# Kernel optimization log

Measured on AMD Instinct MI355X. Metric: run time of the kernel, lower is better.

The kernel has to match this reference:

```python
import jax, jax.numpy as jnp
import numpy as np

B, S, D, H, DFF = 4, 2048, 768, 12, 3072
DH = D // H  # 64
EPS = 1e-5
SQRT_DK = float(np.sqrt(DH))


def layer_norm(x, gamma, beta):
    mu = jnp.mean(x, axis=-1, keepdims=True)
    var = jnp.mean((x - mu) ** 2, axis=-1, keepdims=True)
    return (x - mu) / jnp.sqrt(var + EPS) * gamma + beta


def attention_block(x, Wq, Wv, gamma, beta, mask):
    # NOTE: faithful to source quirks: k and v BOTH come from the V projection
    # (self.K is unused), and softmax is over dim=2 (the QUERY axis) as in
    # nn.Softmax(dim=2) applied to a (B, H, Sq, Sk) tensor.
    b, s, d = x.shape
    q = (x @ Wq).reshape(b, s, H, DH).transpose(0, 2, 1, 3)   # (B,H,S,DH)
    kv = (x @ Wv).reshape(b, s, H, DH).transpose(0, 2, 1, 3)  # (B,H,S,DH)
    w = jnp.einsum('bhqd,bhkd->bhqk', q, kv) / SQRT_DK        # (B,H,S,S)
    w = jnp.where(mask, -1e9, w)
    score = jax.nn.softmax(w, axis=2)  # dim=2 quirk (query axis)
    o = jnp.einsum('bhqk,bhkd->bhqd', score, kv)
    o = o.transpose(0, 2, 1, 3).reshape(b, s, d)
    return layer_norm(o + x, gamma, beta)


def feed_forward(x, W1, b1, W2, b2, gamma, beta):
    h = jax.nn.relu(x @ W1 + b1)
    return layer_norm(h @ W2 + b2 + x, gamma, beta)


def setup_inputs() -> dict:
    key = jax.random.key(0)
    ks = jax.random.split(key, 12)
    std = 1.0 / np.sqrt(D)
    x = jax.random.normal(ks[0], (B, S, D), dtype=jnp.float32)
    # causal mask: True = masked
    mask = jnp.triu(jnp.ones((S, S), dtype=bool), k=1)[None, None]
    return {
        'x': x,
        'mask': mask,
        'Wq1': jax.random.normal(ks[1], (D, D), jnp.float32) * std,
        'Wv1': jax.random.normal(ks[2], (D, D), jnp.float32) * std,
        'g1': jnp.ones((D,), jnp.float32),
        'be1': jnp.zeros((D,), jnp.float32),
        'Wq2': jax.random.normal(ks[3], (D, D), jnp.float32) * std,
        'Wv2': jax.random.normal(ks[4], (D, D), jnp.float32) * std,
        'g2': jnp.ones((D,), jnp.float32),
        'be2': jnp.zeros((D,), jnp.float32),
        'Wf1': jax.random.normal(ks[5], (D, DFF), jnp.float32) * std,
        'bf1': jnp.zeros((DFF,), jnp.float32),
        'Wf2': jax.random.normal(ks[6], (DFF, D), jnp.float32) * (1.0 / np.sqrt(DFF)),
        'bf2': jnp.zeros((D,), jnp.float32),
        'gf': jnp.ones((D,), jnp.float32),
        'bef': jnp.zeros((D,), jnp.float32),
    }


def reference(x, mask, Wq1, Wv1, g1, be1, Wq2, Wv2, g2, be2,
              Wf1, bf1, Wf2, bf2, gf, bef):
    x = attention_block(x, Wq1, Wv1, g1, be1, mask)
    # second block: mask is zeroed in the source (no masking)
    x = attention_block(x, Wq2, Wv2, g2, be2, jnp.zeros_like(mask))
    x = feed_forward(x, Wf1, bf1, Wf2, bf2, gf, bef)
    return x
```

## Files before the change

kernel.cpp:

```cpp
#include <hip/hip_runtime.h>

typedef __attribute__((ext_vector_type(8))) short short8;
typedef __attribute__((ext_vector_type(4))) float floatx4;
typedef __attribute__((ext_vector_type(4))) unsigned short ushort4v;

#define H_ 12
#define S_ 2048
#define D_ 768
#define DFF_ 3072
#define DH_ 64
#define BH_ 48
#define M_ 8192
#define QSCALE 0.180336880f

#if defined(__has_builtin)
#if __has_builtin(__builtin_amdgcn_exp2f)
#define EXP2V(x) __builtin_amdgcn_exp2f(x)
#endif
#if __has_builtin(__builtin_amdgcn_logf)
#define LOG2V(x) __builtin_amdgcn_logf(x)
#endif
#endif
#ifndef EXP2V
#define EXP2V(x) exp2f(x)
#endif
#ifndef LOG2V
#define LOG2V(x) log2f(x)
#endif

__device__ __forceinline__ unsigned short f2bf(float f) {
  union { float f; unsigned int u; } a; a.f = f;
  return (unsigned short)((a.u + 0x7FFFu + ((a.u >> 16) & 1u)) >> 16);
}
__device__ __forceinline__ unsigned int cvtpk_bf16(float lo, float hi) {
  unsigned int u;
  asm("v_cvt_pk_bf16_f32 %0, %1, %2" : "=v"(u) : "v"(lo), "v"(hi));
  return u;
}

__device__ __forceinline__ void glds16(const void* g, void* l) {
  __builtin_amdgcn_global_load_lds(
      (const __attribute__((address_space(1))) void*)(unsigned long long)(size_t)g,
      (__attribute__((address_space(3))) void*)(unsigned int)(size_t)l, 16, 0, 0);
}
__device__ __forceinline__ void glds4(const void* g, void* l) {
  __builtin_amdgcn_global_load_lds(
      (const __attribute__((address_space(1))) void*)(unsigned long long)(size_t)g,
      (__attribute__((address_space(3))) void*)(unsigned int)(size_t)l, 4, 0, 0);
}

__device__ __forceinline__ int swz8(int lin, int nwg) {
  return (lin & 7) * (nwg >> 3) + (lin >> 3);
}

__global__ __launch_bounds__(256) void cvt_bf16(const float* __restrict__ in,
                                                unsigned short* __restrict__ out) {
  size_t i = ((size_t)blockIdx.x * 256 + threadIdx.x) * 4;
  floatx4 v = *reinterpret_cast<const floatx4*>(in + i);
  ushort4v o;
  o[0] = f2bf(v[0]); o[1] = f2bf(v[1]); o[2] = f2bf(v[2]); o[3] = f2bf(v[3]);
  *reinterpret_cast<ushort4v*>(out + i) = o;
}

__global__ __launch_bounds__(256) void wtrans(const float* __restrict__ W,
                                              unsigned short* __restrict__ Wt,
                                              int K, int N) {
  __shared__ float t[64][65];
  const int n0 = blockIdx.x * 64, k0 = blockIdx.y * 64;
  const int tid = threadIdx.x;
#pragma unroll
  for (int i = 0; i < 16; ++i) {
    int idx = tid + 256 * i;
    int kl = idx >> 6, nl = idx & 63;
    t[kl][nl] = W[(size_t)(k0 + kl) * N + n0 + nl];
  }
  __syncthreads();
#pragma unroll
  for (int i = 0; i < 16; ++i) {
    int idx = tid + 256 * i;
    int nl = idx >> 6, kl = idx & 63;
    Wt[(size_t)(n0 + nl) * K + k0 + kl] = f2bf(t[kl][nl]);
  }
}

__global__ __launch_bounds__(256) void kvtrans(const unsigned short* __restrict__ KVb,
                                               unsigned short* __restrict__ KVTb,
                                               unsigned short* __restrict__ kfb) {
  __shared__ unsigned short t[64][72];
  const int kt = blockIdx.x;
  const int kk0 = kt * 64;
  const int bh = blockIdx.y, b = bh / H_, h = bh % H_;
  const size_t xbase = ((size_t)b * S_) * D_ + h * DH_;
  const int tid = threadIdx.x;
#pragma unroll
  for (int i = 0; i < 16; ++i) {
    int idx = tid + 256 * i;
    int kl = idx >> 6, d = idx & 63;
    t[kl][d] = KVb[xbase + (size_t)(kk0 + kl) * D_ + d];
  }
  __syncthreads();
  const size_t tb = (size_t)bh * DH_ * S_;
#pragma unroll
  for (int i = 0; i < 16; ++i) {
    int idx = tid + 256 * i;
    int d = idx >> 6, kl = idx & 63;
    KVTb[tb + (size_t)d * S_ + kk0 + kl] = t[kl][d];
  }
  const size_t obase = ((size_t)bh * 32 + kt) * 4096;
#pragma unroll
  for (int i = 0; i < 2; ++i) {
    int idx = tid + 256 * i;
    int fi = idx >> 6, ll = idx & 63;
    int kkf = fi >> 1, s = fi & 1;
    short8 v =
        *reinterpret_cast<const short8*>(&t[kkf * 16 + (ll & 15)][s * 32 + (ll >> 4) * 8]);
    *reinterpret_cast<short8*>(&kfb[obase + (size_t)fi * 512 + ll * 8]) = v;
  }
}

template <int EPI, int OUTBF>
__global__ __launch_bounds__(256, 2) void gemm128(const unsigned short* __restrict__ A,
                                                  const unsigned short* __restrict__ Bt,
                                                  const float* __restrict__ bias,
                                                  float scale, void* __restrict__ C0,
                                                  void* __restrict__ C1,
                                                  int M, int N, int K, int lda) {
  __shared__ unsigned short As[128 * 64];
  __shared__ unsigned short Bs[128 * 64];
  const int tid = threadIdx.x;
  const int l = tid & 63, w = tid >> 6;
  const int wm = w >> 1, wn = w & 1;
  const int lrow = l & 15, lk = l >> 4;
  int lin = (blockIdx.z * gridDim.y + blockIdx.y) * gridDim.x + blockIdx.x;
  int nwg = gridDim.x * gridDim.y * gridDim.z;
  int s = swz8(lin, nwg);
  int xt = s % gridDim.x;
  int rest = s / gridDim.x;
  int yt = rest % gridDim.y;
  int zt = rest / gridDim.y;
  const unsigned short* Ao = A + (size_t)zt * K;
  const unsigned short* Bo = Bt + (size_t)zt * K;
  const int m0 = yt * 128, n0 = xt * 128;
  floatx4 acc[4][4] = {};
  for (int k0 = 0; k0 < K; k0 += 64) {
    __syncthreads();
#pragma unroll
    for (int i = 0; i < 4; ++i) {
      int idx = w * 64 + i * 256 + l;
      int row = idx >> 3, c8 = idx & 7;
      int sc = (c8 ^ (row & 7)) << 3;
      glds16(Ao + (size_t)(m0 + row) * lda + k0 + sc, As + (size_t)(w * 64 + i * 256) * 8);
      glds16(Bo + (size_t)(n0 + row) * lda + k0 + sc, Bs + (size_t)(w * 64 + i * 256) * 8);
    }
    __syncthreads();
#pragma unroll
    for (int ks = 0; ks < 2; ++ks) {
      short8 af[4], bfr[4];
#pragma unroll
      for (int f = 0; f < 4; ++f) {
        int ar = wm * 64 + f * 16 + lrow;
        af[f] = *reinterpret_cast<const short8*>(
            &As[ar * 64 + (((ks * 4 + lk) ^ (ar & 7)) << 3)]);
        int br = wn * 64 + f * 16 + lrow;
        bfr[f] = *reinterpret_cast<const short8*>(
            &Bs[br * 64 + (((ks * 4 + lk) ^ (br & 7)) << 3)]);
      }
#pragma unroll
      for (int fm = 0; fm < 4; ++fm)
#pragma unroll
        for (int fn = 0; fn < 4; ++fn)
          acc[fm][fn] =
              __builtin_amdgcn_mfma_f32_16x16x32_bf16(af[fm], bfr[fn], acc[fm][fn], 0, 0, 0);
    }
  }
#pragma unroll
  for (int fm = 0; fm < 4; ++fm) {
#pragma unroll
    for (int fn = 0; fn < 4; ++fn) {
      int col = n0 + wn * 64 + fn * 16 + lrow;
#pragma unroll
      for (int r = 0; r < 4; ++r) {
        int row = m0 + wm * 64 + fm * 16 + lk * 4 + r;
        float v = acc[fm][fn][r];
        if (EPI == 3) {
          if (col < 768)
            ((unsigned short*)C0)[(size_t)row * 768 + col] = f2bf(v * scale);
          else
            ((unsigned short*)C1)[(size_t)row * 768 + col - 768] = f2bf(v);
        } else {
          v = v * scale + ((EPI > 0) ? bias[col] : 0.0f);
          if (EPI == 1) v = fmaxf(v, 0.0f);
          void* Cz = zt ? C1 : C0;
          if (OUTBF) ((unsigned short*)Cz)[(size_t)row * N + col] = f2bf(v);
          else ((float*)Cz)[(size_t)row * N + col] = v;
        }
      }
    }
  }
}

template <bool CAUSAL>
__global__ __launch_bounds__(256, 4) void colsum(const unsigned short* __restrict__ Qb,
                                                 const unsigned short* __restrict__ kfb,
                                                 float* __restrict__ lnl) {
  __shared__ float lred[4][64];
  const int tid = threadIdx.x;
  const int l = tid & 63, w = tid >> 6;
  const int lrow = l & 15, lk = l >> 4;
  const int sw = swz8(blockIdx.x, 32 * BH_);
  const int bh = sw >> 5, kt = sw & 31;
  const int kk0 = kt * 64;
  const int b = bh / H_, h = bh % H_;
  const size_t xbase = ((size_t)b * S_) * D_ + h * DH_;
  const unsigned short* kfT = kfb + ((size_t)bh * 32 + kt) * 4096;
  short8 bkv[4][2];
#pragma unroll
  for (int kkf = 0; kkf < 4; ++kkf)
#pragma unroll
    for (int s = 0; s < 2; ++s)
      bkv[kkf][s] =
          *reinterpret_cast<const short8*>(&kfT[(size_t)(kkf * 2 + s) * 512 + l * 8]);
  float lrun[4] = {0.0f, 0.0f, 0.0f, 0.0f};
  const int qbase = CAUSAL ? kk0 : 0;
  const int ntiles = (S_ - qbase) >> 4;
  short8 aqn[2];
  if (w < ntiles) {
    const int q0 = qbase + w * 16;
#pragma unroll
    for (int s = 0; s < 2; ++s)
      aqn[s] = *reinterpret_cast<const short8*>(
          &Qb[xbase + (size_t)(q0 + lrow) * D_ + s * 32 + lk * 8]);
  }
  for (int t = w; t < ntiles; t += 4) {
    const int q0 = qbase + t * 16;
    const bool maskt = CAUSAL && (q0 < kk0 + 64);
    short8 aq0 = aqn[0], aq1 = aqn[1];
    if (t + 4 < ntiles) {
      const int qn = qbase + (t + 4) * 16;
#pragma unroll
      for (int s = 0; s < 2; ++s)
        aqn[s] = *reinterpret_cast<const short8*>(
            &Qb[xbase + (size_t)(qn + lrow) * D_ + s * 32 + lk * 8]);
    }
#pragma unroll
    for (int kkf = 0; kkf < 4; ++kkf) {
      floatx4 sf = {};
      sf = __builtin_amdgcn_mfma_f32_16x16x32_bf16(aq0, bkv[kkf][0], sf, 0, 0, 0);
      sf = __builtin_amdgcn_mfma_f32_16x16x32_bf16(aq1, bkv[kkf][1], sf, 0, 0, 0);
      const int kkg = kk0 + kkf * 16 + lrow;
      float lacc = 0.0f;
      if (maskt) {
#pragma unroll
        for (int r = 0; r < 4; ++r) {
          int qg = q0 + lk * 4 + r;
          lacc += (kkg <= qg) ? EXP2V(sf[r]) : 0.0f;
        }
      } else {
#pragma unroll
        for (int r = 0; r < 4; ++r) lacc += EXP2V(sf[r]);
      }
      lrun[kkf] += lacc;
    }
  }
#pragma unroll
  for (int kkf = 0; kkf < 4; ++kkf) {
    float lv = lrun[kkf];
    lv += __shfl_xor(lv, 16, 64);
    lv += __shfl_xor(lv, 32, 64);
    if (l < 16) lred[w][kkf * 16 + l] = lv;
  }
  __syncthreads();
  if (tid < 64) {
    float lv = lred[0][tid] + lred[1][tid] + lred[2][tid] + lred[3][tid];
    lnl[(size_t)bh * S_ + kk0 + tid] = -LOG2V(lv);
  }
}

template <bool CAUSAL>
__global__ __launch_bounds__(256, 3) void attnpv(const unsigned short* __restrict__ Qb,
                                                 const unsigned short* __restrict__ kfb,
                                                 const unsigned short* __restrict__ KVTb,
                                                 const float* __restrict__ lnl,
                                                 float* __restrict__ Opre) {
  __shared__ unsigned short kvts[2][64 * 64];
  __shared__ float slnl[2][4][64];
  __shared__ unsigned short ps[4][32 * 64];
  const int tid = threadIdx.x;
  const int l = tid & 63, w = tid >> 6;
  const int lrow = l & 15, lk = l >> 4;
  const int sw = swz8(blockIdx.x, 16 * BH_);
  const int bh = sw >> 4, qtr = sw & 15;
  const int qt = CAUSAL ? (15 - qtr) : qtr;
  const int q0 = qt * 128;
  const int wr = w * 32;
  const int b = bh / H_, h = bh % H_;
  const size_t xbase = ((size_t)b * S_) * D_ + h * DH_;
  const size_t tbase = (size_t)bh * DH_ * S_;
  const float* lnlb = lnl + (size_t)bh * S_;
  const unsigned short* kfB = kfb + (size_t)bh * 32 * 4096;

  auto STAGE = [&](int buf, int t) {
    const int kk0 = t * 64;
#pragma unroll
    for (int i = 0; i < 2; ++i) {
      int idx = w * 64 + i * 256 + l;
      int row = idx >> 3, c8 = idx & 7;
      int sc = (c8 ^ (row & 7)) << 3;
      glds16(KVTb + tbase + (size_t)row * S_ + kk0 + sc,
             &kvts[buf][(size_t)(w * 64 + i * 256) * 8]);
    }
    glds4(lnlb + kk0 + l, &slnl[buf][w][0]);
  };

  short8 aq[2][2];
#pragma unroll
  for (int fm = 0; fm < 2; ++fm)
#pragma unroll
    for (int s = 0; s < 2; ++s)
      aq[fm][s] = *reinterpret_cast<const short8*>(
          &Qb[xbase + (size_t)(q0 + wr + fm * 16 + lrow) * D_ + s * 32 + lk * 8]);
  floatx4 ao[2][4] = {};
  const int nkk = CAUSAL ? 2 * (qt + 1) : (S_ / 64);

  STAGE(0, 0);
  int cur = 0;
  for (int t = 0; t < nkk; ++t) {
    const int kk0 = t * 64;
    const bool maskt = CAUSAL && (kk0 + 64 > q0);
    short8 kc[8];
#pragma unroll
    for (int fi = 0; fi < 8; ++fi)
      kc[fi] =
          *reinterpret_cast<const short8*>(&kfB[((size_t)t * 8 + fi) * 512 + l * 8]);
    if (t + 1 < nkk) {
      STAGE(cur ^ 1, t + 1);
      __builtin_amdgcn_sched_barrier(0);
      asm volatile("s_waitcnt vmcnt(11)" ::: "memory");
    } else {
      __builtin_amdgcn_sched_barrier(0);
      asm volatile("s_waitcnt vmcnt(8)" ::: "memory");
    }
    __builtin_amdgcn_s_barrier();
    __builtin_amdgcn_sched_barrier(0);
#pragma unroll
    for (int kkf = 0; kkf < 4; ++kkf) {
      const floatx4 nl4 =
          *reinterpret_cast<const floatx4*>(&slnl[cur][w][kkf * 16 + lk * 4]);
      const int kkbase = kk0 + kkf * 16 + lk * 4;
#pragma unroll
      for (int fm = 0; fm < 2; ++fm) {
        floatx4 sf = nl4;
        sf = __builtin_amdgcn_mfma_f32_16x16x32_bf16(kc[kkf * 2 + 0], aq[fm][0], sf, 0, 0, 0);
        sf = __builtin_amdgcn_mfma_f32_16x16x32_bf16(kc[kkf * 2 + 1], aq[fm][1], sf, 0, 0, 0);
        float p0 = EXP2V(sf[0]);
        float p1 = EXP2V(sf[1]);
        float p2 = EXP2V(sf[2]);
        float p3 = EXP2V(sf[3]);
        if (maskt) {
          const int qg = q0 + wr + fm * 16 + lrow;
          p0 = (kkbase + 0 <= qg) ? p0 : 0.0f;
          p1 = (kkbase + 1 <= qg) ? p1 : 0.0f;
          p2 = (kkbase + 2 <= qg) ? p2 : 0.0f;
          p3 = (kkbase + 3 <= qg) ? p3 : 0.0f;
        }
        unsigned int u0 = cvtpk_bf16(p0, p1);
        unsigned int u1 = cvtpk_bf16(p2, p3);
        const int rowq = fm * 16 + lrow;
        unsigned short* pb =
            &ps[w][rowq * 64 + ((((kkf << 1) + (lk >> 1)) ^ (lrow & 7)) << 3) +
                   ((lk & 1) << 2)];
        *reinterpret_cast<unsigned int*>(pb) = u0;
        *reinterpret_cast<unsigned int*>(pb + 2) = u1;
      }
    }
    short8 pa[2][2];
#pragma unroll
    for (int fm = 0; fm < 2; ++fm)
#pragma unroll
      for (int s2 = 0; s2 < 2; ++s2)
        pa[fm][s2] = *reinterpret_cast<const short8*>(
            &ps[w][(fm * 16 + lrow) * 64 + (((s2 * 4 + lk) ^ (lrow & 7)) << 3)]);
    __builtin_amdgcn_s_setprio(1);
#pragma unroll
    for (int dn = 0; dn < 4; ++dn) {
#pragma unroll
      for (int s2 = 0; s2 < 2; ++s2) {
        const int br2 = dn * 16 + lrow;
        short8 bv = *reinterpret_cast<const short8*>(
            &kvts[cur][br2 * 64 + (((s2 * 4 + lk) ^ (br2 & 7)) << 3)]);
#pragma unroll
        for (int fm = 0; fm < 2; ++fm)
          ao[fm][dn] =
              __builtin_amdgcn_mfma_f32_16x16x32_bf16(pa[fm][s2], bv, ao[fm][dn], 0, 0, 0);
      }
    }
    __builtin_amdgcn_s_setprio(0);
    __builtin_amdgcn_sched_barrier(0);
    __builtin_amdgcn_s_barrier();
    __builtin_amdgcn_sched_barrier(0);
    cur ^= 1;
  }
#pragma unroll
  for (int fm = 0; fm < 2; ++fm)
#pragma unroll
    for (int dn = 0; dn < 4; ++dn)
#pragma unroll
      for (int r = 0; r < 4; ++r)
        Opre[xbase + (size_t)(q0 + wr + fm * 16 + lk * 4 + r) * D_ + dn * 16 + lrow] =
            ao[fm][dn][r];
}

template <bool WRITEBF, bool TWO, bool BIAS>
__global__ __launch_bounds__(256) void ln_kernel(const float* __restrict__ pre,
                                                 const float* __restrict__ pre2,
                                                 const float* __restrict__ bias,
                                                 const float* __restrict__ res,
                                                 const float* __restrict__ gam,
                                                 const float* __restrict__ bet,
                                                 float* __restrict__ outf,
                                                 unsigned short* __restrict__ outb) {
  const int w = threadIdx.x >> 6, l = threadIdx.x & 63;
  const int row = blockIdx.x * 4 + w;
  const size_t base = (size_t)row * D_;
  floatx4 v[3];
  float s = 0.0f;
#pragma unroll
  for (int j = 0; j < 3; ++j) {
    int i = j * 256 + l * 4;
    floatx4 t = *reinterpret_cast<const floatx4*>(&pre[base + i]);
    floatx4 rv = *reinterpret_cast<const floatx4*>(&res[base + i]);
#pragma unroll
    for (int e = 0; e < 4; ++e) t[e] += rv[e];
    if (TWO) {
      floatx4 t2 = *reinterpret_cast<const floatx4*>(&pre2[base + i]);
#pragma unroll
      for (int e = 0; e < 4; ++e) t[e] += t2[e];
    }
    if (BIAS) {
      floatx4 bv = *reinterpret_cast<const floatx4*>(&bias[i]);
#pragma unroll
      for (int e = 0; e < 4; ++e) t[e] += bv[e];
    }
    v[j] = t;
#pragma unroll
    for (int e = 0; e < 4; ++e) s += t[e];
  }
#pragma unroll
  for (int off = 32; off; off >>= 1) s += __shfl_xor(s, off, 64);
  const float mu = s * (1.0f / 768.0f);
  float vs = 0.0f;
#pragma unroll
  for (int j = 0; j < 3; ++j)
#pragma unroll
    for (int e = 0; e < 4; ++e) { float d = v[j][e] - mu; vs += d * d; }
#pragma unroll
  for (int off = 32; off; off >>= 1) vs += __shfl_xor(vs, off, 64);
  const float rstd = rsqrtf(vs * (1.0f / 768.0f) + 1e-5f);
#pragma unroll
  for (int j = 0; j < 3; ++j) {
    int i = j * 256 + l * 4;
    floatx4 gv = *reinterpret_cast<const floatx4*>(&gam[i]);
    floatx4 bev = *reinterpret_cast<const floatx4*>(&bet[i]);
    floatx4 o;
#pragma unroll
    for (int e = 0; e < 4; ++e) o[e] = (v[j][e] - mu) * rstd * gv[e] + bev[e];
    *reinterpret_cast<floatx4*>(&outf[base + i]) = o;
    if (WRITEBF) {
      ushort4v ob;
#pragma unroll
      for (int e = 0; e < 4; ++e) ob[e] = f2bf(o[e]);
      *reinterpret_cast<ushort4v*>(&outb[base + i]) = ob;
    }
  }
}

extern "C" void kernel_launch(void* const* d_in, const int* in_sizes, int n_in,
                              void* d_out, int out_size, void* d_ws, size_t ws_size,
                              hipStream_t stream) {
  const float* x = (const float*)d_in[0];
  const float* Wq1 = (const float*)d_in[2];
  const float* Wv1 = (const float*)d_in[3];
  const float* g1 = (const float*)d_in[4];
  const float* be1 = (const float*)d_in[5];
  const float* Wq2 = (const float*)d_in[6];
  const float* Wv2 = (const float*)d_in[7];
  const float* g2 = (const float*)d_in[8];
  const float* be2 = (const float*)d_in[9];
  const float* Wf1 = (const float*)d_in[10];
  const float* bf1 = (const float*)d_in[11];
  const float* Wf2 = (const float*)d_in[12];
  const float* bf2 = (const float*)d_in[13];
  const float* gf = (const float*)d_in[14];
  const float* bef = (const float*)d_in[15];

  char* ws = (char*)d_ws;
  size_t off = 0;
  auto alloc = [&](size_t bytes) -> void* {
    void* p = ws + off;
    off += (bytes + 255) & ~(size_t)255;
    return p;
  };
  unsigned short* xb = (unsigned short*)alloc((size_t)M_ * D_ * 2);
  unsigned short* qb = (unsigned short*)alloc((size_t)M_ * D_ * 2);
  unsigned short* kvb = (unsigned short*)alloc((size_t)M_ * D_ * 2);
  unsigned short* kvtb = (unsigned short*)alloc((size_t)BH_ * DH_ * S_ * 2);
  unsigned short* kfb = (unsigned short*)alloc((size_t)BH_ * 32 * 4096 * 2);
  float* lnl = (float*)alloc((size_t)BH_ * S_ * 4);
  float* preA = (float*)alloc((size_t)M_ * D_ * 4);
  float* xcur = (float*)alloc((size_t)M_ * D_ * 4);
  unsigned short* hb = (unsigned short*)alloc((size_t)M_ * DFF_ * 2);
  unsigned short* wqv1t = (unsigned short*)alloc((size_t)D_ * 1536 * 2);
  unsigned short* wqv2t = (unsigned short*)alloc((size_t)D_ * 1536 * 2);
  unsigned short* wf1t = (unsigned short*)alloc((size_t)D_ * DFF_ * 2);
  unsigned short* wf2t = (unsigned short*)alloc((size_t)D_ * DFF_ * 2);
  float* preB = (float*)qb;
  if (off > ws_size) return;

  const dim3 blk(256);
  cvt_bf16<<<dim3((M_ * D_) / 1024), blk, 0, stream>>>(x, xb);
  wtrans<<<dim3(12, 12), blk, 0, stream>>>(Wq1, wqv1t, D_, D_);
  wtrans<<<dim3(12, 12), blk, 0, stream>>>(Wv1, wqv1t + (size_t)768 * 768, D_, D_);
  wtrans<<<dim3(12, 12), blk, 0, stream>>>(Wq2, wqv2t, D_, D_);
  wtrans<<<dim3(12, 12), blk, 0, stream>>>(Wv2, wqv2t + (size_t)768 * 768, D_, D_);
  wtrans<<<dim3(48, 12), blk, 0, stream>>>(Wf1, wf1t, D_, DFF_);
  wtrans<<<dim3(12, 48), blk, 0, stream>>>(Wf2, wf2t, DFF_, D_);

  const dim3 gqkv(12, 64);
  const dim3 gkvt(S_ / 64, BH_);

  gemm128<3, 1><<<gqkv, blk, 0, stream>>>(xb, wqv1t, nullptr, QSCALE, qb, kvb, M_, 1536, D_, D_);
  kvtrans<<<gkvt, blk, 0, stream>>>(kvb, kvtb, kfb);
  colsum<true><<<dim3(32 * BH_), blk, 0, stream>>>(qb, kfb, lnl);
  attnpv<true><<<dim3(16 * BH_), blk, 0, stream>>>(qb, kfb, kvtb, lnl, preA);
  ln_kernel<true, false, false><<<dim3(M_ / 4), blk, 0, stream>>>(preA, nullptr, nullptr, x, g1,
                                                                  be1, xcur, xb);

  gemm128<3, 1><<<gqkv, blk, 0, stream>>>(xb, wqv2t, nullptr, QSCALE, qb, kvb, M_, 1536, D_, D_);
  kvtrans<<<gkvt, blk, 0, stream>>>(kvb, kvtb, kfb);
  colsum<false><<<dim3(32 * BH_), blk, 0, stream>>>(qb, kfb, lnl);
  attnpv<false><<<dim3(16 * BH_), blk, 0, stream>>>(qb, kfb, kvtb, lnl, preA);
  ln_kernel<true, false, false><<<dim3(M_ / 4), blk, 0, stream>>>(preA, nullptr, nullptr, xcur,
                                                                  g2, be2, xcur, xb);

  gemm128<1, 1><<<dim3(24, 64), blk, 0, stream>>>(xb, wf1t, bf1, 1.0f, hb, nullptr, M_, DFF_,
                                                  D_, D_);
  gemm128<0, 0><<<dim3(6, 64, 2), blk, 0, stream>>>(hb, wf2t, nullptr, 1.0f, preA, preB, M_, D_,
                                                    DFF_ / 2, DFF_);
  ln_kernel<false, true, true><<<dim3(M_ / 4), blk, 0, stream>>>(preA, preB, bf2, xcur, gf, bef,
                                                                 (float*)d_out, nullptr);
}
```

Baseline: 465.0 us.

## Pre-pack V into MFMA fragment layout and drop LDS staging in attnpv

kvtrans now writes V directly into the per-lane MFMA B-fragment layout instead of a transposed KVT buffer. attnpv loads V fragments and the log-normaliser straight from global memory into registers, removing the LDS double buffer, the async global-to-LDS staging and the two block barriers per tile. This cuts LDS traffic and synchronisation, but loses the explicit prefetch overlap and raises register pressure. Each workgroup now reads the V fragments from global memory or L2 rather than sharing them through LDS.

```diff
diff --git a/kernel.cpp b/kernel.cpp
--- a/kernel.cpp
+++ b/kernel.cpp
@@ -43,11 +43,6 @@
       (const __attribute__((address_space(1))) void*)(unsigned long long)(size_t)g,
       (__attribute__((address_space(3))) void*)(unsigned int)(size_t)l, 16, 0, 0);
 }
-__device__ __forceinline__ void glds4(const void* g, void* l) {
-  __builtin_amdgcn_global_load_lds(
-      (const __attribute__((address_space(1))) void*)(unsigned long long)(size_t)g,
-      (__attribute__((address_space(3))) void*)(unsigned int)(size_t)l, 4, 0, 0);
-}
 
 __device__ __forceinline__ int swz8(int lin, int nwg) {
   return (lin & 7) * (nwg >> 3) + (lin >> 3);
@@ -84,8 +79,8 @@
 }
 
 __global__ __launch_bounds__(256) void kvtrans(const unsigned short* __restrict__ KVb,
-                                               unsigned short* __restrict__ KVTb,
-                                               unsigned short* __restrict__ kfb) {
+                                               unsigned short* __restrict__ kfb,
+                                               unsigned short* __restrict__ vfb) {
   __shared__ unsigned short t[64][72];
   const int kt = blockIdx.x;
   const int kk0 = kt * 64;
@@ -99,13 +94,6 @@
     t[kl][d] = KVb[xbase + (size_t)(kk0 + kl) * D_ + d];
   }
   __syncthreads();
-  const size_t tb = (size_t)bh * DH_ * S_;
-#pragma unroll
-  for (int i = 0; i < 16; ++i) {
-    int idx = tid + 256 * i;
-    int d = idx >> 6, kl = idx & 63;
-    KVTb[tb + (size_t)d * S_ + kk0 + kl] = t[kl][d];
-  }
   const size_t obase = ((size_t)bh * 32 + kt) * 4096;
 #pragma unroll
   for (int i = 0; i < 2; ++i) {
@@ -115,6 +103,17 @@
     short8 v =
         *reinterpret_cast<const short8*>(&t[kkf * 16 + (ll & 15)][s * 32 + (ll >> 4) * 8]);
     *reinterpret_cast<short8*>(&kfb[obase + (size_t)fi * 512 + ll * 8]) = v;
+  }
+#pragma unroll
+  for (int i = 0; i < 2; ++i) {
+    int idx = tid + 256 * i;
+    int fi = idx >> 6, ll = idx & 63;
+    int dn = fi >> 1, s2 = fi & 1;
+    int lrow = ll & 15, lk = ll >> 4;
+    short8 v;
+#pragma unroll
+    for (int j = 0; j < 8; ++j) v[j] = (short)t[(s2 * 4 + lk) * 8 + j][dn * 16 + lrow];
+    *reinterpret_cast<short8*>(&vfb[obase + (size_t)fi * 512 + ll * 8]) = v;
   }
 }
 
@@ -279,11 +278,9 @@
 template <bool CAUSAL>
 __global__ __launch_bounds__(256, 3) void attnpv(const unsigned short* __restrict__ Qb,
                                                  const unsigned short* __restrict__ kfb,
-                                                 const unsigned short* __restrict__ KVTb,
+                                                 const unsigned short* __restrict__ vfb,
                                                  const float* __restrict__ lnl,
                                                  float* __restrict__ Opre) {
-  __shared__ unsigned short kvts[2][64 * 64];
-  __shared__ float slnl[2][4][64];
   __shared__ unsigned short ps[4][32 * 64];
   const int tid = threadIdx.x;
   const int l = tid & 63, w = tid >> 6;
@@ -295,22 +292,9 @@
   const int wr = w * 32;
   const int b = bh / H_, h = bh % H_;
   const size_t xbase = ((size_t)b * S_) * D_ + h * DH_;
-  const size_t tbase = (size_t)bh * DH_ * S_;
   const float* lnlb = lnl + (size_t)bh * S_;
   const unsigned short* kfB = kfb + (size_t)bh * 32 * 4096;
-
-  auto STAGE = [&](int buf, int t) {
-    const int kk0 = t * 64;
-#pragma unroll
-    for (int i = 0; i < 2; ++i) {
-      int idx = w * 64 + i * 256 + l;
-      int row = idx >> 3, c8 = idx & 7;
-      int sc = (c8 ^ (row & 7)) << 3;
-      glds16(KVTb + tbase + (size_t)row * S_ + kk0 + sc,
-             &kvts[buf][(size_t)(w * 64 + i * 256) * 8]);
-    }
-    glds4(lnlb + kk0 + l, &slnl[buf][w][0]);
-  };
+  const unsigned short* vfB = vfb + (size_t)bh * 32 * 4096;
 
   short8 aq[2][2];
 #pragma unroll
@@ -322,34 +306,28 @@
   floatx4 ao[2][4] = {};
   const int nkk = CAUSAL ? 2 * (qt + 1) : (S_ / 64);
 
-  STAGE(0, 0);
-  int cur = 0;
   for (int t = 0; t < nkk; ++t) {
     const int kk0 = t * 64;
     const bool maskt = CAUSAL && (kk0 + 64 > q0);
-    short8 kc[8];
+    const unsigned short* kfT = kfB + (size_t)t * 4096;
+    const unsigned short* vfT = vfB + (size_t)t * 4096;
+    short8 kc[8], vf[8];
 #pragma unroll
     for (int fi = 0; fi < 8; ++fi)
-      kc[fi] =
-          *reinterpret_cast<const short8*>(&kfB[((size_t)t * 8 + fi) * 512 + l * 8]);
-    if (t + 1 < nkk) {
-      STAGE(cur ^ 1, t + 1);
-      __builtin_amdgcn_sched_barrier(0);
-      asm volatile("s_waitcnt vmcnt(11)" ::: "memory");
-    } else {
-      __builtin_amdgcn_sched_barrier(0);
-      asm volatile("s_waitcnt vmcnt(8)" ::: "memory");
-    }
-    __builtin_amdgcn_s_barrier();
-    __builtin_amdgcn_sched_barrier(0);
+      kc[fi] = *reinterpret_cast<const short8*>(&kfT[(size_t)fi * 512 + l * 8]);
+#pragma unroll
+    for (int fi = 0; fi < 8; ++fi)
+      vf[fi] = *reinterpret_cast<const short8*>(&vfT[(size_t)fi * 512 + l * 8]);
+    floatx4 nl[4];
+#pragma unroll
+    for (int kkf = 0; kkf < 4; ++kkf)
+      nl[kkf] = *reinterpret_cast<const floatx4*>(lnlb + kk0 + kkf * 16 + lk * 4);
 #pragma unroll
     for (int kkf = 0; kkf < 4; ++kkf) {
-      const floatx4 nl4 =
-          *reinterpret_cast<const floatx4*>(&slnl[cur][w][kkf * 16 + lk * 4]);
       const int kkbase = kk0 + kkf * 16 + lk * 4;
 #pragma unroll
       for (int fm = 0; fm < 2; ++fm) {
-        floatx4 sf = nl4;
+        floatx4 sf = nl[kkf];
         sf = __builtin_amdgcn_mfma_f32_16x16x32_bf16(kc[kkf * 2 + 0], aq[fm][0], sf, 0, 0, 0);
         sf = __builtin_amdgcn_mfma_f32_16x16x32_bf16(kc[kkf * 2 + 1], aq[fm][1], sf, 0, 0, 0);
         float p0 = EXP2V(sf[0]);
@@ -382,23 +360,14 @@
             &ps[w][(fm * 16 + lrow) * 64 + (((s2 * 4 + lk) ^ (lrow & 7)) << 3)]);
     __builtin_amdgcn_s_setprio(1);
 #pragma unroll
-    for (int dn = 0; dn < 4; ++dn) {
-#pragma unroll
-      for (int s2 = 0; s2 < 2; ++s2) {
-        const int br2 = dn * 16 + lrow;
-        short8 bv = *reinterpret_cast<const short8*>(
-            &kvts[cur][br2 * 64 + (((s2 * 4 + lk) ^ (br2 & 7)) << 3)]);
+    for (int dn = 0; dn < 4; ++dn)
+#pragma unroll
+      for (int s2 = 0; s2 < 2; ++s2)
 #pragma unroll
         for (int fm = 0; fm < 2; ++fm)
-          ao[fm][dn] =
-              __builtin_amdgcn_mfma_f32_16x16x32_bf16(pa[fm][s2], bv, ao[fm][dn], 0, 0, 0);
-      }
-    }
+          ao[fm][dn] = __builtin_amdgcn_mfma_f32_16x16x32_bf16(pa[fm][s2], vf[dn * 2 + s2],
+                                                              ao[fm][dn], 0, 0, 0);
     __builtin_amdgcn_s_setprio(0);
-    __builtin_amdgcn_sched_barrier(0);
-    __builtin_amdgcn_s_barrier();
-    __builtin_amdgcn_sched_barrier(0);
-    cur ^= 1;
   }
 #pragma unroll
   for (int fm = 0; fm < 2; ++fm)
@@ -503,8 +472,8 @@
   unsigned short* xb = (unsigned short*)alloc((size_t)M_ * D_ * 2);
   unsigned short* qb = (unsigned short*)alloc((size_t)M_ * D_ * 2);
   unsigned short* kvb = (unsigned short*)alloc((size_t)M_ * D_ * 2);
-  unsigned short* kvtb = (unsigned short*)alloc((size_t)BH_ * DH_ * S_ * 2);
   unsigned short* kfb = (unsigned short*)alloc((size_t)BH_ * 32 * 4096 * 2);
+  unsigned short* vfb = (unsigned short*)alloc((size_t)BH_ * 32 * 4096 * 2);
   float* lnl = (float*)alloc((size_t)BH_ * S_ * 4);
   float* preA = (float*)alloc((size_t)M_ * D_ * 4);
   float* xcur = (float*)alloc((size_t)M_ * D_ * 4);
@@ -529,16 +498,16 @@
   const dim3 gkvt(S_ / 64, BH_);
 
   gemm128<3, 1><<<gqkv, blk, 0, stream>>>(xb, wqv1t, nullptr, QSCALE, qb, kvb, M_, 1536, D_, D_);
-  kvtrans<<<gkvt, blk, 0, stream>>>(kvb, kvtb, kfb);
+  kvtrans<<<gkvt, blk, 0, stream>>>(kvb, kfb, vfb);
   colsum<true><<<dim3(32 * BH_), blk, 0, stream>>>(qb, kfb, lnl);
-  attnpv<true><<<dim3(16 * BH_), blk, 0, stream>>>(qb, kfb, kvtb, lnl, preA);
+  attnpv<true><<<dim3(16 * BH_), blk, 0, stream>>>(qb, kfb, vfb, lnl, preA);
   ln_kernel<true, false, false><<<dim3(M_ / 4), blk, 0, stream>>>(preA, nullptr, nullptr, x, g1,
                                                                   be1, xcur, xb);
 
   gemm128<3, 1><<<gqkv, blk, 0, stream>>>(xb, wqv2t, nullptr, QSCALE, qb, kvb, M_, 1536, D_, D_);
-  kvtrans<<<gkvt, blk, 0, stream>>>(kvb, kvtb, kfb);
+  kvtrans<<<gkvt, blk, 0, stream>>>(kvb, kfb, vfb);
   colsum<false><<<dim3(32 * BH_), blk, 0, stream>>>(qb, kfb, lnl);
-  attnpv<false><<<dim3(16 * BH_), blk, 0, stream>>>(qb, kfb, kvtb, lnl, preA);
+  attnpv<false><<<dim3(16 * BH_), blk, 0, stream>>>(qb, kfb, vfb, lnl, preA);
   ln_kernel<true, false, false><<<dim3(M_ / 4), blk, 0, stream>>>(preA, nullptr, nullptr, xcur,
                                                                   g2, be2, xcur, xb);
 
```

Result: slower. 479.1 us (+3.0%).
